# Kernel optimization log

Measured on AMD Instinct MI355X. Metric: run time of the kernel, lower is better.

Reference implementation:

```python
import jax, jax.numpy as jnp
import numpy as np

D_MODEL = 3072
NUM_EXPERTS = 8
TOP_K = 2
BATCH, SEQ = 4, 4096


def setup_inputs() -> dict:
    key = jax.random.key(0)
    kx, kw, kb = jax.random.split(key, 3)
    x = jax.random.normal(kx, (BATCH, SEQ, D_MODEL), dtype=jnp.float32)
    W = jax.random.normal(kw, (NUM_EXPERTS, D_MODEL), dtype=jnp.float32) * (1.0 / np.sqrt(D_MODEL))
    b = jax.random.normal(kb, (NUM_EXPERTS,), dtype=jnp.float32) * 0.02
    return {"x": x, "W": W, "b": b}


def reference(x, W, b):
    # Linear gate: [B, S, D] x [E, D]^T -> [B, S, E]
    logits = jnp.einsum("bsd,ed->bse", x, W) + b
    gate_scores = jax.nn.softmax(logits, axis=-1)
    # top-k over experts
    topk_values, topk_indices = jax.lax.top_k(gate_scores, TOP_K)
    # renormalize the selected scores with a second softmax
    topk_values = jax.nn.softmax(topk_values, axis=-1)
    return (topk_values, topk_indices)
```

## Files before the change

### kernel.cpp

```cpp
#include <hip/hip_runtime.h>
#include <stdint.h>


#define NTOK   16384
#define DMODEL 3072
#define NEXP   8
#define NDB    8
#define DCH    (DMODEL / NDB)
#define DS     32
#define NST    (DCH / DS)
#define TPB    256

typedef __attribute__((address_space(1))) const void gvoid;
typedef __attribute__((address_space(3))) void lvoid;

__global__ __launch_bounds__(TPB) void gate_logits_kernel(
    const float* __restrict__ x, const float* __restrict__ W,
    float* __restrict__ logits) {
  __shared__ float4 sx[4][2][512];
  __shared__ float sw[NEXP * DCH];

  const int tid = threadIdx.x;
  const int wv = tid >> 6;
  const int lane = tid & 63;
  const int sl = lane >> 3;
  const int tg = lane & 7;
  const int tokBase = blockIdx.x * TPB;
  const int dBase = blockIdx.y * DCH;

  for (int f = tid; f < NEXP * DCH / 4; f += TPB) {
    const int e = f / (DCH / 4);
    const int j = f % (DCH / 4);
    const float4 v = *(const float4*)&W[e * DMODEL + dBase + j * 4];
    *(float4*)&sw[e * DCH + j * 4] = v;
  }
  __syncthreads();

  const float* xw = x + (size_t)(tokBase + wv * 64) * DMODEL + dBase;

  auto issue = [&](int s, int b) {
    const int d0 = s * DS;
#pragma unroll
    for (int k = 0; k < 8; ++k) {
      const int g = k * 64 + lane;
      const int tok = g >> 3;
      const int slot = g & 7;
      const float* gp = xw + (size_t)tok * DMODEL + d0 + slot * 4;
      __builtin_amdgcn_global_load_lds((gvoid*)gp, (lvoid*)&sx[wv][b][k * 64],
                                       16, 0, 0);
    }
  };

  float acc[8][NEXP];
#pragma unroll
  for (int p = 0; p < 8; ++p)
#pragma unroll
    for (int e = 0; e < NEXP; ++e) acc[p][e] = 0.f;

  issue(0, 0);
  issue(1, 1);

#pragma unroll 2
  for (int s = 0; s < NST; ++s) {
    if (s == NST - 1) {
      asm volatile("s_waitcnt vmcnt(0)" ::: "memory");
    } else {
      asm volatile("s_waitcnt vmcnt(8)" ::: "memory");
    }

    const int b = s & 1;

    float4 w4[NEXP];
#pragma unroll
    for (int e = 0; e < NEXP; ++e)
      w4[e] = *(const float4*)&sw[e * DCH + s * DS + sl * 4];

    const float4* buf = sx[wv][b];
#pragma unroll
    for (int p = 0; p < 8; ++p) {
      const float4 xv = buf[(p * 8 + tg) * 8 + sl];
#pragma unroll
      for (int e = 0; e < NEXP; ++e) {
        acc[p][e] = fmaf(xv.x, w4[e].x,
                    fmaf(xv.y, w4[e].y,
                    fmaf(xv.z, w4[e].z,
                    fmaf(xv.w, w4[e].w, acc[p][e]))));
      }
    }

    if (s + 2 < NST) {
      asm volatile("s_waitcnt lgkmcnt(0)" ::: "memory");
      issue(s + 2, b);
    }
  }

#pragma unroll
  for (int p = 0; p < 8; ++p)
#pragma unroll
    for (int e = 0; e < NEXP; ++e) {
      float v = acc[p][e];
      v += __shfl_xor(v, 8, 64);
      v += __shfl_xor(v, 16, 64);
      v += __shfl_xor(v, 32, 64);
      acc[p][e] = v;
    }

  float out8[NEXP];
#pragma unroll
  for (int p = 0; p < 8; ++p) {
    if (p == sl) {
#pragma unroll
      for (int e = 0; e < NEXP; ++e) out8[e] = acc[p][e];
    }
  }

  float* lp = &logits[(size_t)(tokBase + wv * 64 + lane) * NEXP];
#pragma unroll
  for (int e = 0; e < NEXP; ++e) atomicAdd(lp + e, out8[e]);
}

__global__ __launch_bounds__(64) void gate_topk_kernel(
    const float* __restrict__ logits, const float* __restrict__ bias,
    float* __restrict__ out) {
  const int t = blockIdx.x * 64 + threadIdx.x;
  if (t >= NTOK) return;

  float l[NEXP];
#pragma unroll
  for (int e = 0; e < NEXP; ++e) l[e] = logits[(size_t)t * NEXP + e] + bias[e];

  float m = l[0];
#pragma unroll
  for (int e = 1; e < NEXP; ++e) m = fmaxf(m, l[e]);

  float p[NEXP];
  float ssum = 0.f;
#pragma unroll
  for (int e = 0; e < NEXP; ++e) {
    p[e] = expf(l[e] - m);
    ssum += p[e];
  }
  const float inv = 1.f / ssum;
#pragma unroll
  for (int e = 0; e < NEXP; ++e) p[e] *= inv;

  int i1 = 0;
  float v1 = p[0];
#pragma unroll
  for (int e = 1; e < NEXP; ++e) {
    if (p[e] > v1) { v1 = p[e]; i1 = e; }
  }
  int i2 = -1;
  float v2 = -1.f;
#pragma unroll
  for (int e = 0; e < NEXP; ++e) {
    if (e == i1) continue;
    if (p[e] > v2) { v2 = p[e]; i2 = e; }
  }

  const float e2 = expf(v2 - v1);
  const float r = 1.f / (1.f + e2);

  out[(size_t)t * 2 + 0] = r;
  out[(size_t)t * 2 + 1] = e2 * r;
  out[2 * NTOK + (size_t)t * 2 + 0] = (float)i1;
  out[2 * NTOK + (size_t)t * 2 + 1] = (float)i2;
}

extern "C" void kernel_launch(void* const* d_in, const int* in_sizes, int n_in,
                              void* d_out, int out_size, void* d_ws,
                              size_t ws_size, hipStream_t stream) {
  const float* x = (const float*)d_in[0];
  const float* W = (const float*)d_in[1];
  const float* b = (const float*)d_in[2];
  float* out = (float*)d_out;
  float* logits = (float*)d_ws;

  hipMemsetAsync(d_ws, 0, (size_t)NTOK * NEXP * sizeof(float), stream);

  dim3 grid1(NTOK / TPB, NDB);
  gate_logits_kernel<<<grid1, TPB, 0, stream>>>(x, W, logits);

  gate_topk_kernel<<<NTOK / 64, 64, 0, stream>>>(logits, b, out);
}
```

Baseline: 296.8 us.

## Load x directly into registers and replace atomics with partial-sum buffer

```diff
diff --git a/kernel.cpp b/kernel.cpp
--- a/kernel.cpp
+++ b/kernel.cpp
@@ -11,13 +11,9 @@
 #define NST    (DCH / DS)
 #define TPB    256
 
-typedef __attribute__((address_space(1))) const void gvoid;
-typedef __attribute__((address_space(3))) void lvoid;
-
 __global__ __launch_bounds__(TPB) void gate_logits_kernel(
     const float* __restrict__ x, const float* __restrict__ W,
-    float* __restrict__ logits) {
-  __shared__ float4 sx[4][2][512];
+    float* __restrict__ part) {
   __shared__ float sw[NEXP * DCH];
 
   const int tid = threadIdx.x;
@@ -30,26 +26,17 @@
 
   for (int f = tid; f < NEXP * DCH / 4; f += TPB) {
     const int e = f / (DCH / 4);
-    const int j = f % (DCH / 4);
-    const float4 v = *(const float4*)&W[e * DMODEL + dBase + j * 4];
-    *(float4*)&sw[e * DCH + j * 4] = v;
+    const int j = f - e * (DCH / 4);
+    *(float4*)&sw[e * DCH + j * 4] =
+        *(const float4*)&W[e * DMODEL + dBase + j * 4];
   }
   __syncthreads();
 
-  const float* xw = x + (size_t)(tokBase + wv * 64) * DMODEL + dBase;
-
-  auto issue = [&](int s, int b) {
-    const int d0 = s * DS;
+  const float* p8[8];
 #pragma unroll
-    for (int k = 0; k < 8; ++k) {
-      const int g = k * 64 + lane;
-      const int tok = g >> 3;
-      const int slot = g & 7;
-      const float* gp = xw + (size_t)tok * DMODEL + d0 + slot * 4;
-      __builtin_amdgcn_global_load_lds((gvoid*)gp, (lvoid*)&sx[wv][b][k * 64],
-                                       16, 0, 0);
-    }
-  };
+  for (int p = 0; p < 8; ++p)
+    p8[p] = x + (size_t)(tokBase + wv * 64 + p * 8 + tg) * DMODEL + dBase +
+            sl * 4;
 
   float acc[8][NEXP];
 #pragma unroll
@@ -57,40 +44,51 @@
 #pragma unroll
     for (int e = 0; e < NEXP; ++e) acc[p][e] = 0.f;
 
-  issue(0, 0);
-  issue(1, 1);
+  float4 xa[8], xb[8];
+#pragma unroll
+  for (int p = 0; p < 8; ++p) xa[p] = *(const float4*)(p8[p]);
 
-#pragma unroll 2
-  for (int s = 0; s < NST; ++s) {
-    if (s == NST - 1) {
-      asm volatile("s_waitcnt vmcnt(0)" ::: "memory");
-    } else {
-      asm volatile("s_waitcnt vmcnt(8)" ::: "memory");
-    }
-
-    const int b = s & 1;
+#pragma unroll 1
+  for (int s = 0; s < NST; s += 2) {
+#pragma unroll
+    for (int p = 0; p < 8; ++p)
+      xb[p] = *(const float4*)(p8[p] + (s + 1) * DS);
 
     float4 w4[NEXP];
 #pragma unroll
     for (int e = 0; e < NEXP; ++e)
       w4[e] = *(const float4*)&sw[e * DCH + s * DS + sl * 4];
 
-    const float4* buf = sx[wv][b];
 #pragma unroll
     for (int p = 0; p < 8; ++p) {
-      const float4 xv = buf[(p * 8 + tg) * 8 + sl];
+      const float4 xv = xa[p];
 #pragma unroll
-      for (int e = 0; e < NEXP; ++e) {
+      for (int e = 0; e < NEXP; ++e)
         acc[p][e] = fmaf(xv.x, w4[e].x,
                     fmaf(xv.y, w4[e].y,
                     fmaf(xv.z, w4[e].z,
                     fmaf(xv.w, w4[e].w, acc[p][e]))));
-      }
     }
 
     if (s + 2 < NST) {
-      asm volatile("s_waitcnt lgkmcnt(0)" ::: "memory");
-      issue(s + 2, b);
+#pragma unroll
+      for (int p = 0; p < 8; ++p)
+        xa[p] = *(const float4*)(p8[p] + (s + 2) * DS);
+    }
+
+#pragma unroll
+    for (int e = 0; e < NEXP; ++e)
+      w4[e] = *(const float4*)&sw[e * DCH + (s + 1) * DS + sl * 4];
+
+#pragma unroll
+    for (int p = 0; p < 8; ++p) {
+      const float4 xv = xb[p];
+#pragma unroll
+      for (int e = 0; e < NEXP; ++e)
+        acc[p][e] = fmaf(xv.x, w4[e].x,
+                    fmaf(xv.y, w4[e].y,
+                    fmaf(xv.z, w4[e].z,
+                    fmaf(xv.w, w4[e].w, acc[p][e]))));
     }
   }
 
@@ -114,48 +112,57 @@
     }
   }
 
-  float* lp = &logits[(size_t)(tokBase + wv * 64 + lane) * NEXP];
-#pragma unroll
-  for (int e = 0; e < NEXP; ++e) atomicAdd(lp + e, out8[e]);
+  float* op =
+      part + ((size_t)blockIdx.y * NTOK + tokBase + wv * 64 + lane) * NEXP;
+  *(float4*)op = make_float4(out8[0], out8[1], out8[2], out8[3]);
+  *(float4*)(op + 4) = make_float4(out8[4], out8[5], out8[6], out8[7]);
 }
 
 __global__ __launch_bounds__(64) void gate_topk_kernel(
-    const float* __restrict__ logits, const float* __restrict__ bias,
+    const float* __restrict__ part, const float* __restrict__ bias,
     float* __restrict__ out) {
   const int t = blockIdx.x * 64 + threadIdx.x;
   if (t >= NTOK) return;
 
   float l[NEXP];
 #pragma unroll
-  for (int e = 0; e < NEXP; ++e) l[e] = logits[(size_t)t * NEXP + e] + bias[e];
+  for (int e = 0; e < NEXP; ++e) l[e] = bias[e];
+#pragma unroll
+  for (int p = 0; p < NDB; ++p) {
+    const float* pp = &part[(size_t)p * NTOK * NEXP + (size_t)t * NEXP];
+    const float4 a = *(const float4*)pp;
+    const float4 b = *(const float4*)(pp + 4);
+    l[0] += a.x; l[1] += a.y; l[2] += a.z; l[3] += a.w;
+    l[4] += b.x; l[5] += b.y; l[6] += b.z; l[7] += b.w;
+  }
 
   float m = l[0];
 #pragma unroll
   for (int e = 1; e < NEXP; ++e) m = fmaxf(m, l[e]);
 
-  float p[NEXP];
+  float p8[NEXP];
   float ssum = 0.f;
 #pragma unroll
   for (int e = 0; e < NEXP; ++e) {
-    p[e] = expf(l[e] - m);
-    ssum += p[e];
+    p8[e] = expf(l[e] - m);
+    ssum += p8[e];
   }
   const float inv = 1.f / ssum;
 #pragma unroll
-  for (int e = 0; e < NEXP; ++e) p[e] *= inv;
+  for (int e = 0; e < NEXP; ++e) p8[e] *= inv;
 
   int i1 = 0;
-  float v1 = p[0];
+  float v1 = p8[0];
 #pragma unroll
   for (int e = 1; e < NEXP; ++e) {
-    if (p[e] > v1) { v1 = p[e]; i1 = e; }
+    if (p8[e] > v1) { v1 = p8[e]; i1 = e; }
   }
   int i2 = -1;
   float v2 = -1.f;
 #pragma unroll
   for (int e = 0; e < NEXP; ++e) {
     if (e == i1) continue;
-    if (p[e] > v2) { v2 = p[e]; i2 = e; }
+    if (p8[e] > v2) { v2 = p8[e]; i2 = e; }
   }
 
   const float e2 = expf(v2 - v1);
@@ -174,12 +181,10 @@
   const float* W = (const float*)d_in[1];
   const float* b = (const float*)d_in[2];
   float* out = (float*)d_out;
-  float* logits = (float*)d_ws;
-
-  hipMemsetAsync(d_ws, 0, (size_t)NTOK * NEXP * sizeof(float), stream);
+  float* part = (float*)d_ws;
 
   dim3 grid1(NTOK / TPB, NDB);
-  gate_logits_kernel<<<grid1, TPB, 0, stream>>>(x, W, logits);
+  gate_logits_kernel<<<grid1, TPB, 0, stream>>>(x, W, part);
 
-  gate_topk_kernel<<<NTOK / 64, 64, 0, stream>>>(logits, b, out);
+  gate_topk_kernel<<<NTOK / 64, 64, 0, stream>>>(part, b, out);
 }
```

After: 285.4 us. -3.9%, faster.
